# Kernel optimization log

Hardware: AMD Instinct MI355X
Metric: run time of the kernel (lower is better)

## Reference

```python
import jax, jax.numpy as jnp
import numpy as np

EPS = 1e-9
N = 32768


def signed_area(poly):
    # poly: [..., K, 2] -> signed shoelace area (CCW positive)
    x = poly[..., 0]; y = poly[..., 1]
    x2 = jnp.roll(x, -1, axis=-1); y2 = jnp.roll(y, -1, axis=-1)
    return 0.5 * jnp.sum(x * y2 - x2 * y, axis=-1)


def convex_hull_pad(pts):
    # pts: [K,2] -> [K,2] CCW convex-hull vertices, padded by repeating the last hull vertex.
    K = pts.shape[0]
    a = pts[:, None, None, :]; b = pts[None, :, None, :]; c = pts[None, None, :, :]
    # cr[i,j,k] = cross(p_j - p_i, p_k - p_i); edge i->j on hull iff all points left of it
    cr = (b - a)[..., 0] * (c - a)[..., 1] - (b - a)[..., 1] * (c - a)[..., 0]
    not_eye = ~jnp.eye(K, dtype=bool)
    is_edge = jnp.all(cr >= -1e-7, axis=2) & not_eye
    on_hull = jnp.any(is_edge, axis=1)
    w = on_hull.astype(pts.dtype)
    cen = (pts * w[:, None]).sum(0) / jnp.maximum(w.sum(), 1.0)
    ang = jnp.arctan2(pts[:, 1] - cen[1], pts[:, 0] - cen[0])
    order = jnp.argsort(jnp.where(on_hull, ang, jnp.inf))  # hull verts first, CCW by angle
    sp = pts[order]; sv = on_hull[order]
    last = sp[jnp.maximum(on_hull.sum() - 1, 0)]
    return jnp.where(sv[:, None], sp, last[None, :])


def clip_convex(subject, clip):
    # Sutherland-Hodgman: subject [S,2] CCW polygon (trailing duplicate padding OK),
    # clip [C,2] CCW convex polygon. Fixed-size, jit-friendly.
    S = subject.shape[0]
    poly = subject
    b_all = jnp.roll(clip, -1, axis=0)
    for i in range(clip.shape[0]):  # static small loop over clip edges
        a = clip[i]; b = b_all[i]
        p = poly; q = jnp.roll(poly, -1, axis=0)
        ex = b[0] - a[0]; ey = b[1] - a[1]
        dp = ex * (p[:, 1] - a[1]) - ey * (p[:, 0] - a[0])
        dq = ex * (q[:, 1] - a[1]) - ey * (q[:, 0] - a[0])
        in_p = dp >= 0; in_q = dq >= 0
        denom = dp - dq
        t = dp / jnp.where(jnp.abs(denom) < EPS, EPS, denom)
        inter = p + t[:, None] * (q - p)
        cand = jnp.stack([inter, q], axis=1).reshape(2 * S, 2)
        flags = jnp.stack([in_p != in_q, in_q], axis=1).reshape(2 * S)
        order = jnp.argsort(1 - flags.astype(jnp.int32))  # stable: valid verts first, order kept
        cand = cand[order]; flags = flags[order]
        last = cand[jnp.maximum(flags.sum() - 1, 0)]
        poly = jnp.where(flags[:, None], cand, last[None, :])[:S]
    return poly


def giou_one(pred18, target8):
    P = pred18.reshape(9, 2)
    T = target8.reshape(4, 2)
    sa = signed_area(T)
    T_ccw = jnp.where(sa < 0, T[::-1], T)
    hullA = convex_hull_pad(P)  # [9,2]
    areaA = jnp.abs(signed_area(hullA))
    areaB = jnp.abs(sa)
    # pad subject to 16 verts (clipped 9-gon has <= 13 verts)
    subj = jnp.concatenate([hullA, jnp.broadcast_to(hullA[-1], (7, 2))], axis=0)
    inter = jnp.abs(signed_area(clip_convex(subj, T_ccw)))
    union = areaA + areaB - inter
    hullC = convex_hull_pad(jnp.concatenate([P, T], axis=0))  # enclosing hull of 13 pts
    areaC = jnp.abs(signed_area(hullC))
    return inter / jnp.maximum(union, EPS) - (areaC - union) / jnp.maximum(areaC, EPS)


def setup_inputs():
    key = jax.random.key(0)
    k1, k2, k3, k4, k5, k6 = jax.random.split(key, 6)
    # pred: 9 rep-points scattered around a random center
    ctr = jax.random.uniform(k1, (N, 1, 2), minval=0.0, maxval=1024.0)
    off = jax.random.normal(k2, (N, 9, 2)) * 24.0
    pred = (ctr + off).reshape(N, 18).astype(jnp.float32)
    # target: rotated-rectangle corners [N,8]
    tc = jax.random.uniform(k3, (N, 1, 2), minval=0.0, maxval=1024.0)
    wh = jax.random.uniform(k4, (N, 1, 2), minval=16.0, maxval=128.0)
    ang = jax.random.uniform(k5, (N, 1), minval=0.0, maxval=2.0 * np.pi)
    unit = jnp.array([[-0.5, -0.5], [0.5, -0.5], [0.5, 0.5], [-0.5, 0.5]], jnp.float32)
    xy = unit[None] * wh  # [N,4,2]
    ca = jnp.cos(ang); sn = jnp.sin(ang)
    rx = xy[..., 0] * ca - xy[..., 1] * sn
    ry = xy[..., 0] * sn + xy[..., 1] * ca
    target = (jnp.stack([rx, ry], axis=-1) + tc).reshape(N, 8).astype(jnp.float32)
    weight = jax.random.uniform(k6, (N,), dtype=jnp.float32)
    return {"pred": pred, "target": target, "weight": weight}


def reference(pred, target, weight):
    gious = jax.vmap(giou_one)(pred, target)  # [N]
    loss = (1.0 - gious) * weight
    return jnp.mean(loss)  # reduction='mean', loss_weight=1.0
```

## Files before the change

### kernel.cpp

```cpp
#include <hip/hip_runtime.h>
#include <math.h>

#define EPSF 1e-9f

__global__ __launch_bounds__(256)
void giou_kernel(const float* __restrict__ pred,
                 const float* __restrict__ target,
                 const float* __restrict__ weight,
                 float* __restrict__ out,
                 int n, float invN) {
    __shared__ float2 Hs[13 * 256];
    float2* Hb = &Hs[threadIdx.x];
    const int lane = threadIdx.x;
    const int odd = lane & 1;
    const int i0 = blockIdx.x * 128 + (lane >> 1);
    const bool valid = i0 < n;
    const int i = valid ? i0 : (n > 0 ? n - 1 : 0);

    float Tx[4], Ty[4];
    {
        const float4* tp = (const float4*)target + (size_t)i * 2;
        float4 t0 = tp[0], t1 = tp[1];
        Tx[0] = t0.x; Ty[0] = t0.y; Tx[1] = t0.z; Ty[1] = t0.w;
        Tx[2] = t1.x; Ty[2] = t1.y; Tx[3] = t1.z; Ty[3] = t1.w;
    }
    float w_i = weight[i];
    float ctrx = 0.25f * (Tx[0] + Tx[1] + Tx[2] + Tx[3]);
    float ctry = 0.25f * (Ty[0] + Ty[1] + Ty[2] + Ty[3]);
#pragma unroll
    for (int k = 0; k < 4; k++) { Tx[k] -= ctrx; Ty[k] -= ctry; }

    float saT = 0.5f * ((Tx[0] * Ty[1] - Tx[1] * Ty[0]) + (Tx[1] * Ty[2] - Tx[2] * Ty[1]) +
                        (Tx[2] * Ty[3] - Tx[3] * Ty[2]) + (Tx[3] * Ty[0] - Tx[0] * Ty[3]));
    float areaB = fabsf(saT);
    bool rev = saT < 0.f;
    float tcx[4], tcy[4];
#pragma unroll
    for (int k = 0; k < 4; k++) {
        tcx[k] = rev ? Tx[3 - k] : Tx[k];
        tcy[k] = rev ? Ty[3 - k] : Ty[k];
    }

    float X[13], Y[13];
    {
        const float2* pp = (const float2*)pred + (size_t)i * 9;
#pragma unroll
        for (int k = 0; k < 9; k++) {
            float2 v = pp[k];
            X[k] = v.x - ctrx; Y[k] = v.y - ctry;
        }
    }
#pragma unroll
    for (int k = 0; k < 4; k++) {
        X[9 + k] = odd ? Tx[k] : X[0];
        Y[9 + k] = odd ? Ty[k] : Y[0];
    }

    float sxm = X[0], sym = Y[0];
#pragma unroll
    for (int j = 1; j < 13; j++) {
        bool lt = (X[j] < sxm) || ((X[j] == sxm) && (Y[j] < sym));
        sxm = lt ? X[j] : sxm;
        sym = lt ? Y[j] : sym;
    }
    float cx = sxm, cy = sym;
    float area2 = 0.f;
    int h = 0;
    bool done = false;
#pragma unroll 1
    for (int step = 0; step < 13; step++) {
        if (__builtin_amdgcn_ballot_w64(!done) == 0ull) break;
        float bx = cx, by = cy;
        float db = 0.f;
#pragma unroll
        for (int j = 0; j < 13; j++) {
            float rx = X[j] - cx, ry = Y[j] - cy;
            float dc = rx * rx + ry * ry;
            float ox = bx - cx, oy = by - cy;
            float cr = ox * ry - oy * rx;
            bool rep = (dc > 0.f) &&
                       ((db == 0.f) || (cr < 0.f) || ((cr == 0.f) && (dc > db)));
            bx = rep ? X[j] : bx;
            by = rep ? Y[j] : by;
            db = rep ? dc : db;
        }
        if (!done) {
            Hb[h * 256] = make_float2(cx, cy);
            h++;
            area2 += cx * by - bx * cy;
        }
        done = done || ((bx == sxm) && (by == sym)) || ((bx == cx) && (by == cy));
        cx = bx; cy = by;
    }
    float area = fabsf(0.5f * area2);

    float areaO = __shfl_xor(area, 1, 64);
    float areaA = odd ? areaO : area;
    float areaC = odd ? area : areaO;
    int hO = __shfl_xor(h, 1, 64);
    const int mA = odd ? hO : h;
    __syncthreads();
    const float2* HA = &Hs[lane & ~1];
    float hx[9], hy[9];
#pragma unroll
    for (int j = 0; j < 9; j++) {
        float2 v = HA[j * 256];
        hx[j] = v.x; hy[j] = v.y;
    }

    float S = 0.f;
#pragma unroll
    for (int j = 0; j < 9; j++) {
        bool real_ = (j < mA);
        bool wrapn = (j + 1 < mA);
        float qx_ = wrapn ? hx[(j + 1 < 9) ? j + 1 : 0] : hx[0];
        float qy_ = wrapn ? hy[(j + 1 < 9) ? j + 1 : 0] : hy[0];
        float px_ = hx[j], py_ = hy[j];
        float lo = 0.f, hi = 1.f;
#pragma unroll
        for (int e = 0; e < 4; e++) {
            int e1 = (e + 1) & 3;
            float ex_ = tcx[e1] - tcx[e], ey_ = tcy[e1] - tcy[e];
            float s0 = ex_ * (py_ - tcy[e]) - ey_ * (px_ - tcx[e]);
            float s1 = ex_ * (qy_ - tcy[e]) - ey_ * (qx_ - tcx[e]);
            bool in0 = s0 >= 0.f, in1 = s1 >= 0.f;
            float den = s0 - s1;
            float ddn = (fabsf(den) < 1e-30f) ? 1e-30f : den;
            float t = s0 / ddn;
            bool crs = (in0 != in1);
            lo = (crs && !in0) ? fmaxf(lo, t) : lo;
            hi = (crs && in0)  ? fminf(hi, t) : hi;
            bool out2 = (!in0 && !in1);
            lo = out2 ? 1.f : lo;
            hi = out2 ? 0.f : hi;
        }
        float dxe = qx_ - px_, dye = qy_ - py_;
        float A0x = px_ + lo * dxe, A0y = py_ + lo * dye;
        float B0x = px_ + hi * dxe, B0y = py_ + hi * dye;
        float c_ = A0x * B0y - B0x * A0y;
        S += (real_ && (lo < hi)) ? c_ : 0.f;
    }

    float loT[4] = {0.f, 0.f, 0.f, 0.f}, hiT[4] = {1.f, 1.f, 1.f, 1.f};
#pragma unroll
    for (int j = 0; j < 9; j++) {
        bool pr = (j < mA);
        bool wrapn = (j + 1 < mA);
        float ax_ = hx[j], ay_ = hy[j];
        float bx_ = wrapn ? hx[(j + 1 < 9) ? j + 1 : 0] : hx[0];
        float by_ = wrapn ? hy[(j + 1 < 9) ? j + 1 : 0] : hy[0];
        float ex_ = bx_ - ax_, ey_ = by_ - ay_;
#pragma unroll
        for (int k = 0; k < 4; k++) {
            int k1 = (k + 1) & 3;
            float s0 = ex_ * (tcy[k] - ay_) - ey_ * (tcx[k] - ax_);
            float s1 = ex_ * (tcy[k1] - ay_) - ey_ * (tcx[k1] - ax_);
            bool in0 = s0 >= 0.f, in1 = s1 >= 0.f;
            float den = s0 - s1;
            float ddn = (fabsf(den) < 1e-30f) ? 1e-30f : den;
            float t = s0 / ddn;
            bool crs = (in0 != in1) && pr;
            loT[k] = (crs && !in0) ? fmaxf(loT[k], t) : loT[k];
            hiT[k] = (crs && in0)  ? fminf(hiT[k], t) : hiT[k];
            bool out2 = (!in0 && !in1) && pr;
            loT[k] = out2 ? 1.f : loT[k];
            hiT[k] = out2 ? 0.f : hiT[k];
        }
    }
    bool hullOK = (mA >= 3);
#pragma unroll
    for (int k = 0; k < 4; k++) {
        int k1 = (k + 1) & 3;
        float dxe = tcx[k1] - tcx[k], dye = tcy[k1] - tcy[k];
        float A0x = tcx[k] + loT[k] * dxe, A0y = tcy[k] + loT[k] * dye;
        float B0x = tcx[k] + hiT[k] * dxe, B0y = tcy[k] + hiT[k] * dye;
        float c_ = A0x * B0y - B0x * A0y;
        S += ((loT[k] < hiT[k]) && hullOK) ? c_ : 0.f;
    }
    float inter = fabsf(0.5f * S);

    float uni = areaA + areaB - inter;
    float giou = inter / fmaxf(uni, EPSF) - (areaC - uni) / fmaxf(areaC, EPSF);
    giou = fminf(1.f, fmaxf(-1.f, giou));
    float loss = (1.f - giou) * w_i;
    float contrib = (!odd && valid) ? loss : 0.f;

#pragma unroll
    for (int off = 32; off > 0; off >>= 1) contrib += __shfl_down(contrib, off, 64);
    __shared__ float red[4];
    __syncthreads();
    if ((lane & 63) == 0) red[lane >> 6] = contrib;
    __syncthreads();
    if (lane == 0) {
        float s = red[0] + red[1] + red[2] + red[3];
        atomicAdd(out, s * invN);
    }
}

extern "C" void kernel_launch(void* const* d_in, const int* in_sizes, int n_in,
                              void* d_out, int out_size, void* d_ws, size_t ws_size,
                              hipStream_t stream) {
    const float* pred = (const float*)d_in[0];
    const float* target = (const float*)d_in[1];
    const float* weight = (const float*)d_in[2];
    float* out = (float*)d_out;
    int n = in_sizes[2];

    int grid = (n + 127) / 128;
    giou_kernel<<<grid, 256, 0, stream>>>(pred, target, weight, out, n, 1.0f / (float)n);
}
```

Before: 74.32 us.

## Fuse hull-edge clip loops into one dynamic loop reading hull from LDS

After: 73.82 us. Within noise of the previous version (-0.7%).

```diff
diff --git a/kernel.cpp b/kernel.cpp
--- a/kernel.cpp
+++ b/kernel.cpp
@@ -9,11 +9,11 @@
                  const float* __restrict__ weight,
                  float* __restrict__ out,
                  int n, float invN) {
-    __shared__ float2 Hs[13 * 256];
-    float2* Hb = &Hs[threadIdx.x];
-    const int lane = threadIdx.x;
-    const int odd = lane & 1;
-    const int i0 = blockIdx.x * 128 + (lane >> 1);
+    __shared__ float2 HH[9 * 256];
+    __shared__ float red[4];
+    const int tid = threadIdx.x;
+    const int odd = tid & 1;
+    const int i0 = blockIdx.x * 128 + (tid >> 1);
     const bool valid = i0 < n;
     const int i = valid ? i0 : (n > 0 ? n - 1 : 0);
 
@@ -85,7 +85,7 @@
             db = rep ? dc : db;
         }
         if (!done) {
-            Hb[h * 256] = make_float2(cx, cy);
+            if (!odd && h < 9) HH[h * 256 + tid] = make_float2(cx, cy);
             h++;
             area2 += cx * by - bx * cy;
         }
@@ -98,31 +98,26 @@
     float areaA = odd ? areaO : area;
     float areaC = odd ? area : areaO;
     int hO = __shfl_xor(h, 1, 64);
-    const int mA = odd ? hO : h;
+    int mA = odd ? hO : h;
+    mA = (mA < 9) ? mA : 9;
     __syncthreads();
-    const float2* HA = &Hs[lane & ~1];
-    float hx[9], hy[9];
-#pragma unroll
-    for (int j = 0; j < 9; j++) {
-        float2 v = HA[j * 256];
-        hx[j] = v.x; hy[j] = v.y;
-    }
+    const float2* HP = &HH[tid & ~1];
 
     float S = 0.f;
-#pragma unroll
-    for (int j = 0; j < 9; j++) {
-        bool real_ = (j < mA);
-        bool wrapn = (j + 1 < mA);
-        float qx_ = wrapn ? hx[(j + 1 < 9) ? j + 1 : 0] : hx[0];
-        float qy_ = wrapn ? hy[(j + 1 < 9) ? j + 1 : 0] : hy[0];
-        float px_ = hx[j], py_ = hy[j];
+    float loT[4] = {0.f, 0.f, 0.f, 0.f}, hiT[4] = {1.f, 1.f, 1.f, 1.f};
+#pragma unroll 1
+    for (int j = 0; j < mA; j++) {
+        float2 a = HP[j * 256];
+        int j1 = (j + 1 == mA) ? 0 : j + 1;
+        float2 b = HP[j1 * 256];
+
         float lo = 0.f, hi = 1.f;
 #pragma unroll
         for (int e = 0; e < 4; e++) {
             int e1 = (e + 1) & 3;
             float ex_ = tcx[e1] - tcx[e], ey_ = tcy[e1] - tcy[e];
-            float s0 = ex_ * (py_ - tcy[e]) - ey_ * (px_ - tcx[e]);
-            float s1 = ex_ * (qy_ - tcy[e]) - ey_ * (qx_ - tcx[e]);
+            float s0 = ex_ * (a.y - tcy[e]) - ey_ * (a.x - tcx[e]);
+            float s1 = ex_ * (b.y - tcy[e]) - ey_ * (b.x - tcx[e]);
             bool in0 = s0 >= 0.f, in1 = s1 >= 0.f;
             float den = s0 - s1;
             float ddn = (fabsf(den) < 1e-30f) ? 1e-30f : den;
@@ -134,35 +129,25 @@
             lo = out2 ? 1.f : lo;
             hi = out2 ? 0.f : hi;
         }
-        float dxe = qx_ - px_, dye = qy_ - py_;
-        float A0x = px_ + lo * dxe, A0y = py_ + lo * dye;
-        float B0x = px_ + hi * dxe, B0y = py_ + hi * dye;
-        float c_ = A0x * B0y - B0x * A0y;
-        S += (real_ && (lo < hi)) ? c_ : 0.f;
-    }
+        float dxe = b.x - a.x, dye = b.y - a.y;
+        float A0x = a.x + lo * dxe, A0y = a.y + lo * dye;
+        float B0x = a.x + hi * dxe, B0y = a.y + hi * dye;
+        float c1_ = A0x * B0y - B0x * A0y;
+        S += (lo < hi) ? c1_ : 0.f;
 
-    float loT[4] = {0.f, 0.f, 0.f, 0.f}, hiT[4] = {1.f, 1.f, 1.f, 1.f};
-#pragma unroll
-    for (int j = 0; j < 9; j++) {
-        bool pr = (j < mA);
-        bool wrapn = (j + 1 < mA);
-        float ax_ = hx[j], ay_ = hy[j];
-        float bx_ = wrapn ? hx[(j + 1 < 9) ? j + 1 : 0] : hx[0];
-        float by_ = wrapn ? hy[(j + 1 < 9) ? j + 1 : 0] : hy[0];
-        float ex_ = bx_ - ax_, ey_ = by_ - ay_;
 #pragma unroll
         for (int k = 0; k < 4; k++) {
             int k1 = (k + 1) & 3;
-            float s0 = ex_ * (tcy[k] - ay_) - ey_ * (tcx[k] - ax_);
-            float s1 = ex_ * (tcy[k1] - ay_) - ey_ * (tcx[k1] - ax_);
+            float s0 = dxe * (tcy[k] - a.y) - dye * (tcx[k] - a.x);
+            float s1 = dxe * (tcy[k1] - a.y) - dye * (tcx[k1] - a.x);
             bool in0 = s0 >= 0.f, in1 = s1 >= 0.f;
             float den = s0 - s1;
             float ddn = (fabsf(den) < 1e-30f) ? 1e-30f : den;
             float t = s0 / ddn;
-            bool crs = (in0 != in1) && pr;
+            bool crs = (in0 != in1);
             loT[k] = (crs && !in0) ? fmaxf(loT[k], t) : loT[k];
             hiT[k] = (crs && in0)  ? fminf(hiT[k], t) : hiT[k];
-            bool out2 = (!in0 && !in1) && pr;
+            bool out2 = (!in0 && !in1);
             loT[k] = out2 ? 1.f : loT[k];
             hiT[k] = out2 ? 0.f : hiT[k];
         }
@@ -187,11 +172,10 @@
 
 #pragma unroll
     for (int off = 32; off > 0; off >>= 1) contrib += __shfl_down(contrib, off, 64);
-    __shared__ float red[4];
     __syncthreads();
-    if ((lane & 63) == 0) red[lane >> 6] = contrib;
+    if ((tid & 63) == 0) red[tid >> 6] = contrib;
     __syncthreads();
-    if (lane == 0) {
+    if (tid == 0) {
         float s = red[0] + red[1] + red[2] + red[3];
         atomicAdd(out, s * invN);
     }
```
